# Performance work log

Hardware: AMD Instinct MI355X
Metric: run time of the kernel (lower is better)

## Reference

```python
import jax, jax.numpy as jnp
import numpy as np

N = 50000      # num nodes
E = 800000     # num edges
F_IN = 128     # CONFIG.FeatureLen()
H = 100        # conv1_hide
C = 16         # CONFIG.ClassNum()
LEAKY = 0.01


def setup_inputs() -> dict:
    key = jax.random.key(0)
    k = jax.random.split(key, 4)
    x = jax.random.normal(k[0], (N, F_IN), dtype=jnp.float32)
    edge_index = jax.random.randint(k[1], (2, E), 0, N, dtype=jnp.int32)
    W1 = jax.random.normal(k[2], (F_IN, H), dtype=jnp.float32) / np.sqrt(F_IN).astype(np.float32)
    b1 = jnp.zeros((H,), dtype=jnp.float32)
    W2 = jax.random.normal(k[3], (H, C), dtype=jnp.float32) / np.sqrt(H).astype(np.float32)
    b2 = jnp.zeros((C,), dtype=jnp.float32)
    return {"x": x, "W1": W1, "b1": b1, "W2": W2, "b2": b2, "edge_index": edge_index}


def _gcn_conv(x, W, b, src, dst):
    """PyG GCNConv: x' = D^{-1/2}(A+I)D^{-1/2} X W + b (symmetric norm, self-loops)."""
    x = x @ W  # transform first (smaller feature dim for propagation)
    loop = jnp.arange(N, dtype=src.dtype)
    s = jnp.concatenate([src, loop])  # sources (message senders)
    d = jnp.concatenate([dst, loop])  # targets (message receivers)
    deg = jax.ops.segment_sum(jnp.ones_like(d, dtype=x.dtype), d, num_segments=N)
    dinv = jnp.where(deg > 0, jax.lax.rsqrt(deg), 0.0)
    norm = dinv[s] * dinv[d]                      # [E+N]
    msg = x[s] * norm[:, None]                    # gather + scale
    out = jax.ops.segment_sum(msg, d, num_segments=N)  # scatter-add
    return out + b


def reference(x, W1, b1, W2, b2, edge_index):
    src, dst = edge_index[0], edge_index[1]
    h = _gcn_conv(x, W1, b1, src, dst)
    h = jax.nn.leaky_relu(h, negative_slope=LEAKY)
    # dropout is identity in eval mode (training=False)
    h = _gcn_conv(h, W2, b2, src, dst)
    return jax.nn.log_softmax(h, axis=1)
```

## Files before the change

kernel.cpp:

```cpp
#include <hip/hip_runtime.h>

#define F_IN 128
#define HDIM 100
#define HPAD 128
#define CDIM 16
#define CAP  64
#define BT_STRIDE 136
#define CHUNK 4096
#define KMAX 200
#define RCAP 64

static constexpr float LEAKY = 0.01f;

using short8  = __attribute__((ext_vector_type(8))) short;
using float4v = __attribute__((ext_vector_type(4))) float;
using float2v = __attribute__((ext_vector_type(2))) float;

__device__ __forceinline__ unsigned short f2bf(float f) {
    unsigned u = __float_as_uint(f);
    u += 0x7fffu + ((u >> 16) & 1u);
    return (unsigned short)(u >> 16);
}


__global__ __launch_bounds__(256) void k_gemm1_p1(const float* __restrict__ x,
                                                  const float* __restrict__ W1,
                                                  unsigned char* __restrict__ y1f8,
                                                  const int* __restrict__ src,
                                                  const int* __restrict__ dst,
                                                  unsigned* __restrict__ bkt_edges,
                                                  int* __restrict__ cnt_arr,
                                                  int N, int E, int FB, int KBKT) {
    __shared__ union {
        unsigned short bt[F_IN * BT_STRIDE];
        struct { unsigned stage[CHUNK]; int cnt[KMAX]; } p1;
    } sm;
    int bx = blockIdx.x;
    int t = threadIdx.x;

    if (bx < FB) {
        unsigned* stage = sm.p1.stage;
        int* cnt = sm.p1.cnt;
        for (int i = t; i < KBKT; i += 256) cnt[i] = 0;
        __syncthreads();
        int e0 = bx * CHUNK, e1 = min(E, e0 + CHUNK);
        for (int i = e0 + t; i < e1; i += 256) {
            int d = dst[i];
            unsigned pk = ((unsigned)d << 16) | (unsigned)src[i];
            atomicAdd(&cnt[d >> 8], 1);
            stage[i - e0] = pk;
        }
        __syncthreads();
        for (int i = t; i < KBKT; i += 256) cnt_arr[bx * KBKT + i] = cnt[i];
        __syncthreads();
        for (int i = t; i < KBKT; i += 256) cnt[i] = 0;
        __syncthreads();
        int m = e1 - e0;
        for (int i = t; i < m; i += 256) {
            unsigned pk = stage[i];
            int b = pk >> 24;
            int pos = atomicAdd(&cnt[b], 1);
            if (pos < RCAP)
                bkt_edges[((size_t)b * FB + bx) * RCAP + pos] = pk;
        }
        return;
    }

    for (int idx = t; idx < F_IN * HPAD; idx += 256) {
        int k = idx >> 7;
        int n = idx & 127;
        float v = (n < HDIM) ? W1[k * HDIM + n] : 0.f;
        sm.bt[n * BT_STRIDE + k] = f2bf(v);
    }
    __syncthreads();

    int wave = t >> 6, lane = t & 63;
    int Mtiles = (N + 15) >> 4;
    int tile = (bx - FB) * 4 + wave;
    if (tile >= Mtiles) return;
    int row0 = tile * 16;

    int m = lane & 15;
    int kq = lane >> 4;
    int arow = min(row0 + m, N - 1);
    const float* xrow = x + (size_t)arow * F_IN;

    short8 afrag[4];
    #pragma unroll
    for (int kt = 0; kt < 4; ++kt) {
        int kb = kt * 32 + kq * 8;
        float4 a0 = *(const float4*)(xrow + kb);
        float4 a1 = *(const float4*)(xrow + kb + 4);
        short8 f;
        f[0] = (short)f2bf(a0.x); f[1] = (short)f2bf(a0.y);
        f[2] = (short)f2bf(a0.z); f[3] = (short)f2bf(a0.w);
        f[4] = (short)f2bf(a1.x); f[5] = (short)f2bf(a1.y);
        f[6] = (short)f2bf(a1.z); f[7] = (short)f2bf(a1.w);
        afrag[kt] = f;
    }

    bool full = (row0 + 15 < N);
    #pragma unroll
    for (int ct = 0; ct < 8; ++ct) {
        float4v acc = {0.f, 0.f, 0.f, 0.f};
        #pragma unroll
        for (int kt = 0; kt < 4; ++kt) {
            short8 b = *(const short8*)&sm.bt[(ct * 16 + m) * BT_STRIDE + kt * 32 + kq * 8];
            acc = __builtin_amdgcn_mfma_f32_16x16x32_bf16(afrag[kt], b, acc, 0, 0, 0);
        }
        #pragma unroll
        for (int i = 0; i < 4; ++i) {
            int r = row0 + kq * 4 + i;
            int v8 = __builtin_amdgcn_cvt_pk_fp8_f32(acc[i], acc[i], 0, false);
            if (full || r < N)
                y1f8[(size_t)r * HPAD + ct * 16 + m] = (unsigned char)(v8 & 0xff);
        }
    }
}


__global__ __launch_bounds__(256) void k_p2(const unsigned* __restrict__ bkt_edges,
                                            const int* __restrict__ cnt_arr,
                                            int* __restrict__ deg,
                                            unsigned short* __restrict__ slots,
                                            int N, int FB, int KBKT) {
    __shared__ int cur[256];
    int b = blockIdx.x, t = threadIdx.x;
    cur[t] = 0;
    __syncthreads();
    for (int fb = t; fb < FB; fb += 256) {
        int c = cnt_arr[fb * KBKT + b];
        size_t base = ((size_t)b * FB + fb) * RCAP;
        for (int j = 0; j < c; ++j) {
            unsigned pk = bkt_edges[base + j];
            int d = pk >> 16;
            int pos = atomicAdd(&cur[d & 255], 1);
            if (pos < CAP)
                slots[(size_t)d * CAP + pos] = (unsigned short)(pk & 0xffffu);
        }
    }
    __syncthreads();
    int n = (b << 8) + t;
    if (n < N) deg[n] = cur[t];
}


__global__ __launch_bounds__(256) void k_agg1y2(const unsigned* __restrict__ y1u,
                                                const float* __restrict__ b1,
                                                const float* __restrict__ W2,
                                                const int* __restrict__ deg,
                                                const unsigned short* __restrict__ slots,
                                                float* __restrict__ y2, int N) {
    __shared__ float W2s[HDIM * CDIM];
    __shared__ float hs[4][2][HPAD];
    int t = threadIdx.x;
    for (int idx = t; idx < HDIM * CDIM; idx += 256) W2s[idx] = W2[idx];
    __syncthreads();

    int wave = t >> 6, lane = t & 63;
    int half = lane >> 5, l = lane & 31;
    int hbase = lane & 32;
    int n = blockIdx.x * 8 + wave * 2 + half;
    bool valid = (n < N);
    int nn = valid ? n : (N - 1);

    int beg = nn * CAP;
    int cnt = valid ? deg[nn] : 0;
    float dn = rsqrtf((float)deg[nn] + 1.0f);

    int cother = __shfl(cnt, lane ^ 32);
    int cmax = max(cnt, cother);

    float a0 = 0.f, a1 = 0.f, a2 = 0.f, a3 = 0.f;
    for (int e0 = 0; e0 < cmax; e0 += 32) {
        int mm = min(32, cnt - e0);
        unsigned su = 0u; float wv = 0.f;
        if (l < mm) {
            su = slots[beg + e0 + l];
            wv = rsqrtf((float)deg[su] + 1.0f);
        }
        int mmax = min(32, cmax - e0);
        int mpad = (mmax + 7) & ~7;
        for (int j = 0; j < mpad; j += 8) {
            float w[8]; unsigned vv[8];
            #pragma unroll
            for (int q = 0; q < 8; ++q) {
                int ln = hbase | (j + q);
                unsigned s = (unsigned)__shfl((int)su, ln);
                w[q] = __shfl(wv, ln);
                vv[q] = y1u[(size_t)s * 32 + l];
            }
            #pragma unroll
            for (int q = 0; q < 8; ++q) {
                float2v lov = __builtin_amdgcn_cvt_pk_f32_fp8((int)vv[q], false);
                float2v hiv = __builtin_amdgcn_cvt_pk_f32_fp8((int)vv[q], true);
                a0 = fmaf(w[q], lov[0], a0);
                a1 = fmaf(w[q], lov[1], a1);
                a2 = fmaf(w[q], hiv[0], a2);
                a3 = fmaf(w[q], hiv[1], a3);
            }
        }
    }
    {
        unsigned vn = y1u[(size_t)nn * 32 + l];
        float2v lov = __builtin_amdgcn_cvt_pk_f32_fp8((int)vn, false);
        float2v hiv = __builtin_amdgcn_cvt_pk_f32_fp8((int)vn, true);
        a0 = fmaf(dn, lov[0], a0);
        a1 = fmaf(dn, lov[1], a1);
        a2 = fmaf(dn, hiv[0], a2);
        a3 = fmaf(dn, hiv[1], a3);
    }

    float4 bb = (l < 25) ? *(const float4*)&b1[4 * l] : make_float4(0.f, 0.f, 0.f, 0.f);
    float h0 = fmaf(dn, a0, bb.x);
    float h1 = fmaf(dn, a1, bb.y);
    float h2 = fmaf(dn, a2, bb.z);
    float h3 = fmaf(dn, a3, bb.w);
    h0 = h0 > 0.f ? h0 : LEAKY * h0;
    h1 = h1 > 0.f ? h1 : LEAKY * h1;
    h2 = h2 > 0.f ? h2 : LEAKY * h2;
    h3 = h3 > 0.f ? h3 : LEAKY * h3;
    *(float4*)&hs[wave][half][4 * l] = make_float4(h0, h1, h2, h3);
    __builtin_amdgcn_wave_barrier();

    int c = l & 15, kg = l >> 4;
    const float* hrow = hs[wave][half];
    float p = 0.f;
    #pragma unroll 10
    for (int j = 0; j < 50; ++j) {
        int k = 2 * j + kg;
        p = fmaf(hrow[k], W2s[k * CDIM + c], p);
    }
    p += __shfl_down(p, 16);
    if (l < 16 && valid) y2[(size_t)n * CDIM + c] = p;
}


__global__ __launch_bounds__(256) void k_agg2(const float* __restrict__ y2,
                                              const float* __restrict__ b2,
                                              const int* __restrict__ deg,
                                              const unsigned short* __restrict__ slots,
                                              float* __restrict__ out, int N) {
    int t = threadIdx.x;
    int wave = t >> 6, lane = t & 63;
    int sub = lane >> 4, c = lane & 15;
    int n = blockIdx.x * 16 + wave * 4 + sub;
    bool valid = (n < N);
    int nn = valid ? n : 0;

    int beg = nn * CAP;
    int cnt = valid ? deg[nn] : 0;
    float dn = rsqrtf((float)deg[nn] + 1.0f);
    float acc = dn * y2[(size_t)nn * CDIM + c];

    for (int e0 = 0; e0 < cnt; e0 += 16) {
        int mm = min(16, cnt - e0);
        unsigned su = 0u; float wv = 0.f;
        if (c < mm) {
            su = slots[beg + e0 + c];
            wv = rsqrtf((float)deg[su] + 1.0f);
        }
        int mpad = (mm + 3) & ~3;
        for (int j = 0; j < mpad; j += 4) {
            float w[4]; float v[4];
            #pragma unroll
            for (int q = 0; q < 4; ++q) {
                int ln = sub * 16 + j + q;
                unsigned s = (unsigned)__shfl((int)su, ln);
                w[q] = __shfl(wv, ln);
                v[q] = y2[(size_t)s * CDIM + c];
            }
            #pragma unroll
            for (int q = 0; q < 4; ++q) acc = fmaf(w[q], v[q], acc);
        }
    }

    float lg = fmaf(dn, acc, b2[c]);
    float mx = lg;
    #pragma unroll
    for (int k = 8; k; k >>= 1) mx = fmaxf(mx, __shfl_xor(mx, k));
    float ex = __expf(lg - mx);
    #pragma unroll
    for (int k = 8; k; k >>= 1) ex += __shfl_xor(ex, k);
    float lse = mx + __logf(ex);
    if (valid) out[(size_t)n * CDIM + c] = lg - lse;
}


extern "C" void kernel_launch(void* const* d_in, const int* in_sizes, int n_in,
                              void* d_out, int out_size, void* d_ws, size_t ws_size,
                              hipStream_t stream) {
    const float* x  = (const float*)d_in[0];
    const float* W1 = (const float*)d_in[1];
    const float* b1 = (const float*)d_in[2];
    const float* W2 = (const float*)d_in[3];
    const float* b2 = (const float*)d_in[4];
    const int*   ei = (const int*)d_in[5];

    const int N = in_sizes[0] / F_IN;
    const int E = in_sizes[5] / 2;
    const int* src = ei;
    const int* dst = ei + E;

    const int KBKT = (N + 255) >> 8;
    const int FB   = (E + CHUNK - 1) / CHUNK;

    char* ws = (char*)d_ws;
    size_t off = 0;
    auto alloc = [&](size_t bytes) {
        char* p = ws + off;
        off += (bytes + 255) & ~(size_t)255;
        return p;
    };
    int*            deg       = (int*)alloc((size_t)N * 4);
    unsigned char*  y1f8      = (unsigned char*)alloc((size_t)N * HPAD);
    float*          y2        = (float*)alloc((size_t)N * CDIM * 4);
    unsigned short* slots     = (unsigned short*)alloc((size_t)N * CAP * 2);
    int*            cnt_arr   = (int*)alloc((size_t)FB * KBKT * 4);
    unsigned*       bkt_edges = (unsigned*)alloc((size_t)KBKT * FB * RCAP * 4);
    (void)ws_size; (void)n_in; (void)out_size;

    int Mtiles = (N + 15) / 16;
    int GG = (Mtiles + 3) / 4;

    k_gemm1_p1<<<FB + GG, 256, 0, stream>>>(x, W1, y1f8, src, dst,
                                            bkt_edges, cnt_arr, N, E, FB, KBKT);
    k_p2<<<KBKT, 256, 0, stream>>>(bkt_edges, cnt_arr, deg, slots, N, FB, KBKT);
    k_agg1y2<<<(N + 7) / 8, 256, 0, stream>>>((const unsigned*)y1f8, b1, W2,
                                              deg, slots, y2, N);
    k_agg2<<<(N + 15) / 16, 256, 0, stream>>>(y2, b2, deg, slots,
                                              (float*)d_out, N);
}
```

Measured before the change: 163.7 us.

## Build per-node adjacency in LDS from 32-node buckets inside aggregation kernels

Buckets edges by 32-node destination groups instead of 256-node groups, with a smaller per-chunk capacity, and drops the global slots CSR array. Each aggregation kernel rebuilds its block's adjacency lists in shared memory from the bucketed edges, and a separate lightweight kernel computes only degrees. This removes the global slots write and read traffic and scatters the CSR fill across blocks. The cost is that the bucket scan is done twice (once per layer), the RCAP=24 and CAP=64 truncations can drop edges when buckets overflow, and KMAX grows to 1600, which enlarges shared memory in the first kernel.

```diff
diff --git a/kernel.cpp b/kernel.cpp
--- a/kernel.cpp
+++ b/kernel.cpp
@@ -5,10 +5,11 @@
 #define HPAD 128
 #define CDIM 16
 #define CAP  64
+#define NB   32
 #define BT_STRIDE 136
 #define CHUNK 4096
-#define KMAX 200
-#define RCAP 64
+#define KMAX 1600
+#define RCAP 24
 
 static constexpr float LEAKY = 0.01f;
 
@@ -47,7 +48,7 @@
         for (int i = e0 + t; i < e1; i += 256) {
             int d = dst[i];
             unsigned pk = ((unsigned)d << 16) | (unsigned)src[i];
-            atomicAdd(&cnt[d >> 8], 1);
+            atomicAdd(&cnt[d >> 5], 1);
             stage[i - e0] = pk;
         }
         __syncthreads();
@@ -58,7 +59,7 @@
         int m = e1 - e0;
         for (int i = t; i < m; i += 256) {
             unsigned pk = stage[i];
-            int b = pk >> 24;
+            int b = pk >> 21;
             int pos = atomicAdd(&cnt[b], 1);
             if (pos < RCAP)
                 bkt_edges[((size_t)b * FB + bx) * RCAP + pos] = pk;
@@ -119,29 +120,25 @@
 }
 
 
-__global__ __launch_bounds__(256) void k_p2(const unsigned* __restrict__ bkt_edges,
-                                            const int* __restrict__ cnt_arr,
-                                            int* __restrict__ deg,
-                                            unsigned short* __restrict__ slots,
-                                            int N, int FB, int KBKT) {
-    __shared__ int cur[256];
+__global__ __launch_bounds__(256) void k_deg2(const unsigned* __restrict__ bkt_edges,
+                                              const int* __restrict__ cnt_arr,
+                                              int* __restrict__ deg,
+                                              int N, int FB, int KBKT) {
+    __shared__ int cur[NB];
     int b = blockIdx.x, t = threadIdx.x;
-    cur[t] = 0;
+    if (t < NB) cur[t] = 0;
     __syncthreads();
     for (int fb = t; fb < FB; fb += 256) {
-        int c = cnt_arr[fb * KBKT + b];
+        int c = min(cnt_arr[fb * KBKT + b], RCAP);
         size_t base = ((size_t)b * FB + fb) * RCAP;
         for (int j = 0; j < c; ++j) {
             unsigned pk = bkt_edges[base + j];
-            int d = pk >> 16;
-            int pos = atomicAdd(&cur[d & 255], 1);
-            if (pos < CAP)
-                slots[(size_t)d * CAP + pos] = (unsigned short)(pk & 0xffffu);
-        }
-    }
-    __syncthreads();
-    int n = (b << 8) + t;
-    if (n < N) deg[n] = cur[t];
+            atomicAdd(&cur[(pk >> 16) & (NB - 1)], 1);
+        }
+    }
+    __syncthreads();
+    int n = b * NB + t;
+    if (t < NB && n < N) deg[n] = cur[t];
 }
 
 
@@ -149,141 +146,186 @@
                                                 const float* __restrict__ b1,
                                                 const float* __restrict__ W2,
                                                 const int* __restrict__ deg,
-                                                const unsigned short* __restrict__ slots,
-                                                float* __restrict__ y2, int N) {
+                                                const unsigned* __restrict__ bkt_edges,
+                                                const int* __restrict__ cnt_arr,
+                                                float* __restrict__ y2,
+                                                int N, int FB, int KBKT) {
     __shared__ float W2s[HDIM * CDIM];
+    __shared__ float b1s[HPAD];
     __shared__ float hs[4][2][HPAD];
-    int t = threadIdx.x;
+    __shared__ unsigned short slotsL[NB * CAP];
+    __shared__ int cur[NB];
+    int b = blockIdx.x, t = threadIdx.x;
+    int n0 = b * NB;
+
     for (int idx = t; idx < HDIM * CDIM; idx += 256) W2s[idx] = W2[idx];
+    if (t < HPAD) b1s[t] = (t < HDIM) ? b1[t] : 0.f;
+    if (t < NB) cur[t] = 0;
+    __syncthreads();
+
+    for (int fb = t; fb < FB; fb += 256) {
+        int c = min(cnt_arr[fb * KBKT + b], RCAP);
+        size_t base = ((size_t)b * FB + fb) * RCAP;
+        for (int j = 0; j < c; ++j) {
+            unsigned pk = bkt_edges[base + j];
+            int loc = (pk >> 16) & (NB - 1);
+            int pos = atomicAdd(&cur[loc], 1);
+            if (pos < CAP)
+                slotsL[loc * CAP + pos] = (unsigned short)(pk & 0xffffu);
+        }
+    }
     __syncthreads();
 
     int wave = t >> 6, lane = t & 63;
     int half = lane >> 5, l = lane & 31;
     int hbase = lane & 32;
-    int n = blockIdx.x * 8 + wave * 2 + half;
-    bool valid = (n < N);
-    int nn = valid ? n : (N - 1);
-
-    int beg = nn * CAP;
-    int cnt = valid ? deg[nn] : 0;
-    float dn = rsqrtf((float)deg[nn] + 1.0f);
-
-    int cother = __shfl(cnt, lane ^ 32);
-    int cmax = max(cnt, cother);
-
-    float a0 = 0.f, a1 = 0.f, a2 = 0.f, a3 = 0.f;
-    for (int e0 = 0; e0 < cmax; e0 += 32) {
-        int mm = min(32, cnt - e0);
-        unsigned su = 0u; float wv = 0.f;
-        if (l < mm) {
-            su = slots[beg + e0 + l];
-            wv = rsqrtf((float)deg[su] + 1.0f);
-        }
-        int mmax = min(32, cmax - e0);
-        int mpad = (mmax + 7) & ~7;
-        for (int j = 0; j < mpad; j += 8) {
-            float w[8]; unsigned vv[8];
-            #pragma unroll
-            for (int q = 0; q < 8; ++q) {
-                int ln = hbase | (j + q);
-                unsigned s = (unsigned)__shfl((int)su, ln);
-                w[q] = __shfl(wv, ln);
-                vv[q] = y1u[(size_t)s * 32 + l];
+    for (int pass = 0; pass < 4; ++pass) {
+        int loc = pass * 8 + wave * 2 + half;
+        int n = n0 + loc;
+        bool valid = (n < N);
+        int nn = valid ? n : (N - 1);
+        int cnt = cur[loc];
+        float dn = rsqrtf((float)cnt + 1.0f);
+
+        int cother = __shfl(cnt, lane ^ 32);
+        int cmax = max(cnt, cother);
+
+        float a0 = 0.f, a1 = 0.f, a2 = 0.f, a3 = 0.f;
+        for (int e0 = 0; e0 < cmax; e0 += 32) {
+            int mm = min(32, cnt - e0);
+            unsigned su = 0u; float wv = 0.f;
+            if (l < mm) {
+                su = slotsL[loc * CAP + e0 + l];
+                wv = rsqrtf((float)deg[su] + 1.0f);
             }
-            #pragma unroll
-            for (int q = 0; q < 8; ++q) {
-                float2v lov = __builtin_amdgcn_cvt_pk_f32_fp8((int)vv[q], false);
-                float2v hiv = __builtin_amdgcn_cvt_pk_f32_fp8((int)vv[q], true);
-                a0 = fmaf(w[q], lov[0], a0);
-                a1 = fmaf(w[q], lov[1], a1);
-                a2 = fmaf(w[q], hiv[0], a2);
-                a3 = fmaf(w[q], hiv[1], a3);
+            int mmax = min(32, cmax - e0);
+            int mpad = (mmax + 7) & ~7;
+            for (int j = 0; j < mpad; j += 8) {
+                float w[8]; unsigned vv[8];
+                #pragma unroll
+                for (int q = 0; q < 8; ++q) {
+                    int ln = hbase | (j + q);
+                    unsigned s = (unsigned)__shfl((int)su, ln);
+                    w[q] = __shfl(wv, ln);
+                    vv[q] = y1u[(size_t)s * 32 + l];
+                }
+                #pragma unroll
+                for (int q = 0; q < 8; ++q) {
+                    float2v lov = __builtin_amdgcn_cvt_pk_f32_fp8((int)vv[q], false);
+                    float2v hiv = __builtin_amdgcn_cvt_pk_f32_fp8((int)vv[q], true);
+                    a0 = fmaf(w[q], lov[0], a0);
+                    a1 = fmaf(w[q], lov[1], a1);
+                    a2 = fmaf(w[q], hiv[0], a2);
+                    a3 = fmaf(w[q], hiv[1], a3);
+                }
             }
         }
-    }
-    {
-        unsigned vn = y1u[(size_t)nn * 32 + l];
-        float2v lov = __builtin_amdgcn_cvt_pk_f32_fp8((int)vn, false);
-        float2v hiv = __builtin_amdgcn_cvt_pk_f32_fp8((int)vn, true);
-        a0 = fmaf(dn, lov[0], a0);
-        a1 = fmaf(dn, lov[1], a1);
-        a2 = fmaf(dn, hiv[0], a2);
-        a3 = fmaf(dn, hiv[1], a3);
-    }
-
-    float4 bb = (l < 25) ? *(const float4*)&b1[4 * l] : make_float4(0.f, 0.f, 0.f, 0.f);
-    float h0 = fmaf(dn, a0, bb.x);
-    float h1 = fmaf(dn, a1, bb.y);
-    float h2 = fmaf(dn, a2, bb.z);
-    float h3 = fmaf(dn, a3, bb.w);
-    h0 = h0 > 0.f ? h0 : LEAKY * h0;
-    h1 = h1 > 0.f ? h1 : LEAKY * h1;
-    h2 = h2 > 0.f ? h2 : LEAKY * h2;
-    h3 = h3 > 0.f ? h3 : LEAKY * h3;
-    *(float4*)&hs[wave][half][4 * l] = make_float4(h0, h1, h2, h3);
-    __builtin_amdgcn_wave_barrier();
-
-    int c = l & 15, kg = l >> 4;
-    const float* hrow = hs[wave][half];
-    float p = 0.f;
-    #pragma unroll 10
-    for (int j = 0; j < 50; ++j) {
-        int k = 2 * j + kg;
-        p = fmaf(hrow[k], W2s[k * CDIM + c], p);
-    }
-    p += __shfl_down(p, 16);
-    if (l < 16 && valid) y2[(size_t)n * CDIM + c] = p;
+        {
+            unsigned vn = y1u[(size_t)nn * 32 + l];
+            float2v lov = __builtin_amdgcn_cvt_pk_f32_fp8((int)vn, false);
+            float2v hiv = __builtin_amdgcn_cvt_pk_f32_fp8((int)vn, true);
+            a0 = fmaf(dn, lov[0], a0);
+            a1 = fmaf(dn, lov[1], a1);
+            a2 = fmaf(dn, hiv[0], a2);
+            a3 = fmaf(dn, hiv[1], a3);
+        }
+        float4 bb = (l < 25) ? *(const float4*)&b1s[4 * l] : make_float4(0.f, 0.f, 0.f, 0.f);
+        float h0 = fmaf(dn, a0, bb.x);
+        float h1 = fmaf(dn, a1, bb.y);
+        float h2 = fmaf(dn, a2, bb.z);
+        float h3 = fmaf(dn, a3, bb.w);
+        h0 = h0 > 0.f ? h0 : LEAKY * h0;
+        h1 = h1 > 0.f ? h1 : LEAKY * h1;
+        h2 = h2 > 0.f ? h2 : LEAKY * h2;
+        h3 = h3 > 0.f ? h3 : LEAKY * h3;
+        *(float4*)&hs[wave][half][4 * l] = make_float4(h0, h1, h2, h3);
+        __builtin_amdgcn_wave_barrier();
+
+        int c = l & 15, kg = l >> 4;
+        const float* hrow = hs[wave][half];
+        float p = 0.f;
+        #pragma unroll 10
+        for (int j = 0; j < 50; ++j) {
+            int k = 2 * j + kg;
+            p = fmaf(hrow[k], W2s[k * CDIM + c], p);
+        }
+        p += __shfl_down(p, 16);
+        if (l < 16 && valid) y2[(size_t)n * CDIM + c] = p;
+    }
 }
 
 
 __global__ __launch_bounds__(256) void k_agg2(const float* __restrict__ y2,
                                               const float* __restrict__ b2,
                                               const int* __restrict__ deg,
-                                              const unsigned short* __restrict__ slots,
-                                              float* __restrict__ out, int N) {
-    int t = threadIdx.x;
+                                              const unsigned* __restrict__ bkt_edges,
+                                              const int* __restrict__ cnt_arr,
+                                              float* __restrict__ out,
+                                              int N, int FB, int KBKT) {
+    __shared__ unsigned short slotsL[NB * CAP];
+    __shared__ int cur[NB];
+    int b = blockIdx.x, t = threadIdx.x;
+    int n0 = b * NB;
+    if (t < NB) cur[t] = 0;
+    __syncthreads();
+
+    for (int fb = t; fb < FB; fb += 256) {
+        int c = min(cnt_arr[fb * KBKT + b], RCAP);
+        size_t base = ((size_t)b * FB + fb) * RCAP;
+        for (int j = 0; j < c; ++j) {
+            unsigned pk = bkt_edges[base + j];
+            int loc = (pk >> 16) & (NB - 1);
+            int pos = atomicAdd(&cur[loc], 1);
+            if (pos < CAP)
+                slotsL[loc * CAP + pos] = (unsigned short)(pk & 0xffffu);
+        }
+    }
+    __syncthreads();
+
     int wave = t >> 6, lane = t & 63;
     int sub = lane >> 4, c = lane & 15;
-    int n = blockIdx.x * 16 + wave * 4 + sub;
-    bool valid = (n < N);
-    int nn = valid ? n : 0;
-
-    int beg = nn * CAP;
-    int cnt = valid ? deg[nn] : 0;
-    float dn = rsqrtf((float)deg[nn] + 1.0f);
-    float acc = dn * y2[(size_t)nn * CDIM + c];
-
-    for (int e0 = 0; e0 < cnt; e0 += 16) {
-        int mm = min(16, cnt - e0);
-        unsigned su = 0u; float wv = 0.f;
-        if (c < mm) {
-            su = slots[beg + e0 + c];
-            wv = rsqrtf((float)deg[su] + 1.0f);
-        }
-        int mpad = (mm + 3) & ~3;
-        for (int j = 0; j < mpad; j += 4) {
-            float w[4]; float v[4];
-            #pragma unroll
-            for (int q = 0; q < 4; ++q) {
-                int ln = sub * 16 + j + q;
-                unsigned s = (unsigned)__shfl((int)su, ln);
-                w[q] = __shfl(wv, ln);
-                v[q] = y2[(size_t)s * CDIM + c];
+    float b2c = b2[c];
+    for (int pass = 0; pass < 2; ++pass) {
+        int loc = pass * 16 + wave * 4 + sub;
+        int n = n0 + loc;
+        bool valid = (n < N);
+        int nn = valid ? n : 0;
+        int cnt = valid ? cur[loc] : 0;
+        float dn = rsqrtf((float)cur[loc] + 1.0f);
+        float acc = dn * y2[(size_t)nn * CDIM + c];
+
+        for (int e0 = 0; e0 < cnt; e0 += 16) {
+            int mm = min(16, cnt - e0);
+            unsigned su = 0u; float wv = 0.f;
+            if (c < mm) {
+                su = slotsL[loc * CAP + e0 + c];
+                wv = rsqrtf((float)deg[su] + 1.0f);
             }
-            #pragma unroll
-            for (int q = 0; q < 4; ++q) acc = fmaf(w[q], v[q], acc);
-        }
-    }
-
-    float lg = fmaf(dn, acc, b2[c]);
-    float mx = lg;
-    #pragma unroll
-    for (int k = 8; k; k >>= 1) mx = fmaxf(mx, __shfl_xor(mx, k));
-    float ex = __expf(lg - mx);
-    #pragma unroll
-    for (int k = 8; k; k >>= 1) ex += __shfl_xor(ex, k);
-    float lse = mx + __logf(ex);
-    if (valid) out[(size_t)n * CDIM + c] = lg - lse;
+            int mpad = (mm + 3) & ~3;
+            for (int j = 0; j < mpad; j += 4) {
+                float w[4]; float v[4];
+                #pragma unroll
+                for (int q = 0; q < 4; ++q) {
+                    int ln = (sub << 4) + j + q;
+                    unsigned s = (unsigned)__shfl((int)su, ln);
+                    w[q] = __shfl(wv, ln);
+                    v[q] = y2[(size_t)s * CDIM + c];
+                }
+                #pragma unroll
+                for (int q = 0; q < 4; ++q) acc = fmaf(w[q], v[q], acc);
+            }
+        }
+
+        float lg = fmaf(dn, acc, b2c);
+        float mx = lg;
+        #pragma unroll
+        for (int k = 8; k; k >>= 1) mx = fmaxf(mx, __shfl_xor(mx, k));
+        float ex = __expf(lg - mx);
+        #pragma unroll
+        for (int k = 8; k; k >>= 1) ex += __shfl_xor(ex, k);
+        float lse = mx + __logf(ex);
+        if (valid) out[(size_t)n * CDIM + c] = lg - lse;
+    }
 }
 
 
@@ -297,13 +339,13 @@
     const float* b2 = (const float*)d_in[4];
     const int*   ei = (const int*)d_in[5];
 
-    const int N = in_sizes[0] / F_IN;
-    const int E = in_sizes[5] / 2;
+    int N = in_sizes[0] / F_IN;
+    int E = in_sizes[5] / 2;
     const int* src = ei;
     const int* dst = ei + E;
 
-    const int KBKT = (N + 255) >> 8;
-    const int FB   = (E + CHUNK - 1) / CHUNK;
+    int KBKT = (N + NB - 1) / NB;
+    int FB   = (E + CHUNK - 1) / CHUNK;
 
     char* ws = (char*)d_ws;
     size_t off = 0;
@@ -315,7 +357,6 @@
     int*            deg       = (int*)alloc((size_t)N * 4);
     unsigned char*  y1f8      = (unsigned char*)alloc((size_t)N * HPAD);
     float*          y2        = (float*)alloc((size_t)N * CDIM * 4);
-    unsigned short* slots     = (unsigned short*)alloc((size_t)N * CAP * 2);
     int*            cnt_arr   = (int*)alloc((size_t)FB * KBKT * 4);
     unsigned*       bkt_edges = (unsigned*)alloc((size_t)KBKT * FB * RCAP * 4);
     (void)ws_size; (void)n_in; (void)out_size;
@@ -325,9 +366,9 @@
 
     k_gemm1_p1<<<FB + GG, 256, 0, stream>>>(x, W1, y1f8, src, dst,
                                             bkt_edges, cnt_arr, N, E, FB, KBKT);
-    k_p2<<<KBKT, 256, 0, stream>>>(bkt_edges, cnt_arr, deg, slots, N, FB, KBKT);
-    k_agg1y2<<<(N + 7) / 8, 256, 0, stream>>>((const unsigned*)y1f8, b1, W2,
-                                              deg, slots, y2, N);
-    k_agg2<<<(N + 15) / 16, 256, 0, stream>>>(y2, b2, deg, slots,
-                                              (float*)d_out, N);
-}
+    k_deg2<<<KBKT, 256, 0, stream>>>(bkt_edges, cnt_arr, deg, N, FB, KBKT);
+    k_agg1y2<<<KBKT, 256, 0, stream>>>((const unsigned*)y1f8, b1, W2, deg,
+                                       bkt_edges, cnt_arr, y2, N, FB, KBKT);
+    k_agg2<<<KBKT, 256, 0, stream>>>(y2, b2, deg, bkt_edges, cnt_arr,
+                                     (float*)d_out, N, FB, KBKT);
+}
```

Result: slower. 171.6 us (+4.8%).
